# Optimization experiments

Measured on AMD Instinct MI355X. Metric: run time of the kernel, lower is better.

Reference implementation:

```python
import jax, jax.numpy as jnp
import numpy as np

B, S, H, F, E, TOPK = 2, 1024, 1024, 2816, 8, 2

def setup_inputs() -> dict:
    key = jax.random.key(0)
    k1, k2, k3, k4 = jax.random.split(key, 4)
    return {
        "hidden_states": jax.random.normal(k1, (B, S, H), dtype=jnp.float32),
        "gate_w": jax.random.normal(k2, (E, H), dtype=jnp.float32) * 0.02,  # gate 1x1 conv == [E,H] matrix
        "w1": jax.random.normal(k3, (E, F, H), dtype=jnp.float32) * 0.02,   # per-expert up-proj
        "w2": jax.random.normal(k4, (E, H, F), dtype=jnp.float32) * 0.02,   # per-expert down-proj
        "top_k": TOPK,
    }

def reference(hidden_states, gate_w, w1, w2, top_k):
    b, s, h = hidden_states.shape
    e = gate_w.shape[0]
    x = hidden_states.reshape(-1, h)                       # [N, H]
    n = x.shape[0]
    # Router: 1x1 conv gate == linear, softmax, top-k, renormalize
    logits = x @ gate_w.T                                  # [N, E]
    probs = jax.nn.softmax(logits, axis=-1)
    topw, topi = jax.lax.top_k(probs, top_k)               # [N, k]
    topw = topw / jnp.sum(topw, axis=-1, keepdims=True)
    # Per-(token, expert) combine weight; zero for non-selected experts.
    # Equivalent to torch.where(topk_indices == e, topk_weights, 0).sum(-1).
    comb = jnp.zeros((n, e), dtype=x.dtype).at[jnp.arange(n)[:, None], topi].add(topw)  # [N, E]
    # Expert MLPs (1x1 convs == GEMMs): up -> SiLU -> down, weighted combine.
    up = jnp.einsum('nh,efh->nef', x, w1)                  # [N, E, F]
    act = jax.nn.silu(up)
    out = jnp.einsum('nef,ehf->neh', act, w2)              # [N, E, H]
    y = jnp.einsum('ne,neh->nh', comb, out)                # weighted combine
    return y.reshape(b, s, h)
```

## Files before the change

kernel.cpp:

```cpp
#include <hip/hip_runtime.h>
#include <stdint.h>

#define N_TOK 2048
#define H_DIM 1024
#define F_DIM 2816
#define N_EXP 8
#define NSLOT (N_TOK * 2)

#define BK 64
#define KSPLIT 2
#define KHALF (F_DIM / KSPLIT)

#define N8_X (N_TOK * H_DIM / 8)
#define N8_W (N_EXP * F_DIM * H_DIM / 8)

typedef __attribute__((ext_vector_type(8))) short bf16x8;
typedef __attribute__((ext_vector_type(4))) float f32x4;

typedef __attribute__((address_space(1))) unsigned int gu32;
typedef __attribute__((address_space(3))) unsigned int lu32;

static __device__ __forceinline__ unsigned short f2bf(float f) {
    union { float f; unsigned u; } v; v.f = f;
    unsigned r = v.u + 0x7fffu + ((v.u >> 16) & 1u);
    return (unsigned short)(r >> 16);
}

static __device__ __forceinline__ void gload16(const unsigned short* g, unsigned short* l) {
    __builtin_amdgcn_global_load_lds((const gu32*)g, (lu32*)l, 16, 0, 0);
}

__global__ __launch_bounds__(256) void convert_all_kernel(
    const float* __restrict__ x, const float* __restrict__ w1, const float* __restrict__ w2,
    unsigned short* __restrict__ x_bf, unsigned short* __restrict__ w1_bf, unsigned short* __restrict__ w2_bf)
{
    const int total = N8_X + 2 * N8_W;
    int i = blockIdx.x * 256 + threadIdx.x;
    const int stride = gridDim.x * 256;
    for (; i < total; i += stride) {
        const float* src; unsigned short* dst; size_t k;
        if (i < N8_X)            { src = x;  dst = x_bf;  k = i; }
        else if (i < N8_X + N8_W){ src = w1; dst = w1_bf; k = i - N8_X; }
        else                     { src = w2; dst = w2_bf; k = i - N8_X - N8_W; }
        const float4 a = *(const float4*)(src + k * 8);
        const float4 b = *(const float4*)(src + k * 8 + 4);
        ushort4 lo, hi;
        lo.x = f2bf(a.x); lo.y = f2bf(a.y); lo.z = f2bf(a.z); lo.w = f2bf(a.w);
        hi.x = f2bf(b.x); hi.y = f2bf(b.y); hi.z = f2bf(b.z); hi.w = f2bf(b.w);
        uint4 out;
        out.x = (unsigned)lo.x | ((unsigned)lo.y << 16);
        out.y = (unsigned)lo.z | ((unsigned)lo.w << 16);
        out.z = (unsigned)hi.x | ((unsigned)hi.y << 16);
        out.w = (unsigned)hi.z | ((unsigned)hi.w << 16);
        *(uint4*)(dst + k * 8) = out;
    }
}

__global__ __launch_bounds__(256) void router_kernel(
    const float* __restrict__ x, const float* __restrict__ gate_w,
    int* __restrict__ counts, int* __restrict__ row_token, float* __restrict__ row_weight,
    int* __restrict__ slot_e, int* __restrict__ slot_pos)
{
    __shared__ float gsm[N_EXP * H_DIM];
    for (int i = threadIdx.x; i < N_EXP * H_DIM; i += 256) gsm[i] = gate_w[i];
    __syncthreads();

    const int wave = threadIdx.x >> 6;
    const int lane = threadIdx.x & 63;
    const int n = blockIdx.x * 4 + wave;
    if (n >= N_TOK) return;

    float xv[16];
#pragma unroll
    for (int i = 0; i < 16; i++) xv[i] = x[(size_t)n * H_DIM + lane + 64 * i];

    float logit[N_EXP];
#pragma unroll
    for (int e = 0; e < N_EXP; e++) {
        float p = 0.f;
#pragma unroll
        for (int i = 0; i < 16; i++) p += xv[i] * gsm[e * H_DIM + lane + 64 * i];
#pragma unroll
        for (int s = 32; s > 0; s >>= 1) p += __shfl_xor(p, s, 64);
        logit[e] = p;
    }

    if (lane == 0) {
        int e0 = 0; float l0 = logit[0];
#pragma unroll
        for (int e = 1; e < N_EXP; e++) if (logit[e] > l0) { l0 = logit[e]; e0 = e; }
        int e1 = -1; float l1 = -3.4e38f;
#pragma unroll
        for (int e = 0; e < N_EXP; e++) if (e != e0 && logit[e] > l1) { l1 = logit[e]; e1 = e; }
        float w0 = 1.f / (1.f + __expf(l1 - l0));
        float w1 = 1.f - w0;
        int p0 = atomicAdd(&counts[e0], 1);
        int p1 = atomicAdd(&counts[e1], 1);
        row_token[e0 * N_TOK + p0] = n;  row_weight[e0 * N_TOK + p0] = w0;
        row_token[e1 * N_TOK + p1] = n;  row_weight[e1 * N_TOK + p1] = w1;
        slot_e[n * 2 + 0] = e0;  slot_pos[n * 2 + 0] = p0;
        slot_e[n * 2 + 1] = e1;  slot_pos[n * 2 + 1] = p1;
    }
}

__global__ void scan_kernel(const int* __restrict__ counts, int* __restrict__ offsets)
{
    if (threadIdx.x == 0 && blockIdx.x == 0) {
        int acc = 0;
        for (int e = 0; e < N_EXP; e++) { offsets[e] = acc; acc += counts[e]; }
    }
}

__global__ __launch_bounds__(256) void up_gemm_kernel(
    const unsigned short* __restrict__ x_bf, const unsigned short* __restrict__ w1_bf,
    const int* __restrict__ counts, const int* __restrict__ offsets,
    const int* __restrict__ row_token,
    unsigned short* __restrict__ act)
{
    const int e = blockIdx.z;
    const int cnt = counts[e];
    const int mTile = blockIdx.y;
    if (mTile * 128 >= cnt) return;
    const int fTile = blockIdx.x;
    const int off = offsets[e];

    __shared__ __align__(16) unsigned short As[128 * 64];
    __shared__ __align__(16) unsigned short Bs[128 * 64];

    const int tid = threadIdx.x;
    const int lane = tid & 63;
    const int wave = tid >> 6;
    const int wm = (wave >> 1) * 64, wn = (wave & 1) * 64;

    const unsigned short* aSrc[4];
    const unsigned short* bSrc[4];
#pragma unroll
    for (int j = 0; j < 4; j++) {
        const int row_local = wave * 32 + j * 8 + (lane >> 3);
        const int pos = mTile * 128 + row_local;
        const int tok = row_token[e * N_TOK + min(pos, cnt - 1)];
        aSrc[j] = x_bf + (size_t)tok * H_DIM + (lane & 7) * 8;
        bSrc[j] = w1_bf + ((size_t)e * F_DIM + fTile * 128 + row_local) * H_DIM + (lane & 7) * 8;
    }

    f32x4 acc[4][4];
#pragma unroll
    for (int i = 0; i < 4; i++)
#pragma unroll
        for (int j = 0; j < 4; j++) acc[i][j] = (f32x4)(0.f);

    const int NKT = H_DIM / BK;
    for (int kt = 0; kt < NKT; kt++) {
        const int koff = kt * BK;
#pragma unroll
        for (int j = 0; j < 4; j++) {
            gload16(aSrc[j] + koff, As + (wave * 4 + j) * 512);
            gload16(bSrc[j] + koff, Bs + (wave * 4 + j) * 512);
        }
        __syncthreads();
#pragma unroll
        for (int kk = 0; kk < BK / 32; kk++) {
            const int kloc = kk * 32 + (lane >> 4) * 8;
            bf16x8 af[4], bfr[4];
#pragma unroll
            for (int i = 0; i < 4; i++)
                af[i] = *(const bf16x8*)(As + (wm + i * 16 + (lane & 15)) * 64 + kloc);
#pragma unroll
            for (int i = 0; i < 4; i++)
                bfr[i] = *(const bf16x8*)(Bs + (wn + i * 16 + (lane & 15)) * 64 + kloc);
#pragma unroll
            for (int i = 0; i < 4; i++)
#pragma unroll
                for (int j = 0; j < 4; j++)
                    acc[i][j] = __builtin_amdgcn_mfma_f32_16x16x32_bf16(af[i], bfr[j], acc[i][j], 0, 0, 0);
        }
        __syncthreads();
    }

#pragma unroll
    for (int i = 0; i < 4; i++) {
        const int mrow = wm + i * 16 + ((lane >> 4) << 2);
#pragma unroll
        for (int r = 0; r < 4; r++) {
            const int m = mTile * 128 + mrow + r;
            if (m < cnt) {
#pragma unroll
                for (int j = 0; j < 4; j++) {
                    float v = acc[i][j][r];
                    float s = v / (1.f + __expf(-v));
                    int col = fTile * 128 + wn + j * 16 + (lane & 15);
                    act[(size_t)(off + m) * F_DIM + col] = f2bf(s);
                }
            }
        }
    }
}

__global__ __launch_bounds__(256) void down_gemm_kernel(
    const unsigned short* __restrict__ act, const unsigned short* __restrict__ w2_bf,
    const int* __restrict__ counts, const int* __restrict__ offsets,
    const float* __restrict__ row_weight,
    float* __restrict__ out_partial)
{
    const int e  = blockIdx.z & (N_EXP - 1);
    const int ks = blockIdx.z >> 3;
    const int cnt = counts[e];
    const int mTile = blockIdx.y;
    if (mTile * 128 >= cnt) return;
    const int hTile = blockIdx.x;
    const int off = offsets[e];
    const int kbase = ks * KHALF;

    __shared__ __align__(16) unsigned short As[128 * 64];
    __shared__ __align__(16) unsigned short Bs[128 * 64];

    const int tid = threadIdx.x;
    const int lane = tid & 63;
    const int wave = tid >> 6;
    const int wm = (wave >> 1) * 64, wn = (wave & 1) * 64;

    const unsigned short* aSrc[4];
    const unsigned short* bSrc[4];
#pragma unroll
    for (int j = 0; j < 4; j++) {
        const int row_local = wave * 32 + j * 8 + (lane >> 3);
        const int slot = off + min(mTile * 128 + row_local, cnt - 1);
        aSrc[j] = act + (size_t)slot * F_DIM + kbase + (lane & 7) * 8;
        bSrc[j] = w2_bf + ((size_t)e * H_DIM + hTile * 128 + row_local) * F_DIM + kbase + (lane & 7) * 8;
    }

    f32x4 acc[4][4];
#pragma unroll
    for (int i = 0; i < 4; i++)
#pragma unroll
        for (int j = 0; j < 4; j++) acc[i][j] = (f32x4)(0.f);

    const int NKT = KHALF / BK;
    for (int kt = 0; kt < NKT; kt++) {
        const int koff = kt * BK;
#pragma unroll
        for (int j = 0; j < 4; j++) {
            gload16(aSrc[j] + koff, As + (wave * 4 + j) * 512);
            gload16(bSrc[j] + koff, Bs + (wave * 4 + j) * 512);
        }
        __syncthreads();
#pragma unroll
        for (int kk = 0; kk < BK / 32; kk++) {
            const int kloc = kk * 32 + (lane >> 4) * 8;
            bf16x8 af[4], bfr[4];
#pragma unroll
            for (int i = 0; i < 4; i++)
                af[i] = *(const bf16x8*)(As + (wm + i * 16 + (lane & 15)) * 64 + kloc);
#pragma unroll
            for (int i = 0; i < 4; i++)
                bfr[i] = *(const bf16x8*)(Bs + (wn + i * 16 + (lane & 15)) * 64 + kloc);
#pragma unroll
            for (int i = 0; i < 4; i++)
#pragma unroll
                for (int j = 0; j < 4; j++)
                    acc[i][j] = __builtin_amdgcn_mfma_f32_16x16x32_bf16(af[i], bfr[j], acc[i][j], 0, 0, 0);
        }
        __syncthreads();
    }

    float* obase = out_partial + (size_t)ks * NSLOT * H_DIM;
#pragma unroll
    for (int i = 0; i < 4; i++) {
        const int mrow = wm + i * 16 + ((lane >> 4) << 2);
#pragma unroll
        for (int r = 0; r < 4; r++) {
            const int m = mTile * 128 + mrow + r;
            if (m < cnt) {
                const float w = row_weight[e * N_TOK + m];
#pragma unroll
                for (int j = 0; j < 4; j++) {
                    int col = hTile * 128 + wn + j * 16 + (lane & 15);
                    obase[(size_t)(off + m) * H_DIM + col] = w * acc[i][j][r];
                }
            }
        }
    }
}

__global__ __launch_bounds__(256) void combine_kernel(
    const float* __restrict__ out_partial, const int* __restrict__ offsets,
    const int* __restrict__ slot_e, const int* __restrict__ slot_pos,
    float* __restrict__ out)
{
    const int n = blockIdx.x;
    const int r0 = offsets[slot_e[n * 2 + 0]] + slot_pos[n * 2 + 0];
    const int r1 = offsets[slot_e[n * 2 + 1]] + slot_pos[n * 2 + 1];
    const int t = threadIdx.x;
    const float* p0 = out_partial;
    const float* p1 = out_partial + (size_t)NSLOT * H_DIM;
    const float4 a = *(const float4*)(p0 + (size_t)r0 * H_DIM + t * 4);
    const float4 b = *(const float4*)(p1 + (size_t)r0 * H_DIM + t * 4);
    const float4 c = *(const float4*)(p0 + (size_t)r1 * H_DIM + t * 4);
    const float4 d = *(const float4*)(p1 + (size_t)r1 * H_DIM + t * 4);
    float4 s;
    s.x = (a.x + b.x) + (c.x + d.x);
    s.y = (a.y + b.y) + (c.y + d.y);
    s.z = (a.z + b.z) + (c.z + d.z);
    s.w = (a.w + b.w) + (c.w + d.w);
    *(float4*)(out + (size_t)n * H_DIM + t * 4) = s;
}

extern "C" void kernel_launch(void* const* d_in, const int* in_sizes, int n_in,
                              void* d_out, int out_size, void* d_ws, size_t ws_size,
                              hipStream_t stream) {
    const float* x      = (const float*)d_in[0];
    const float* gate_w = (const float*)d_in[1];
    const float* w1     = (const float*)d_in[2];
    const float* w2     = (const float*)d_in[3];
    float* out = (float*)d_out;

    char* ws = (char*)d_ws;
    size_t o = 0;
    auto alloc = [&](size_t bytes) -> void* {
        void* p = ws + o;
        o = (o + bytes + 255) & ~(size_t)255;
        return p;
    };
    int*   counts     = (int*)  alloc(N_EXP * sizeof(int));
    int*   offsets    = (int*)  alloc(N_EXP * sizeof(int));
    int*   row_token  = (int*)  alloc((size_t)N_EXP * N_TOK * sizeof(int));
    float* row_weight = (float*)alloc((size_t)N_EXP * N_TOK * sizeof(float));
    int*   slot_e     = (int*)  alloc((size_t)N_TOK * 2 * sizeof(int));
    int*   slot_pos   = (int*)  alloc((size_t)N_TOK * 2 * sizeof(int));
    unsigned short* act = (unsigned short*)alloc((size_t)NSLOT * F_DIM * sizeof(unsigned short));
    float* out_partial = (float*)alloc((size_t)KSPLIT * NSLOT * H_DIM * sizeof(float));
    unsigned short* x_bf  = (unsigned short*)alloc((size_t)N_TOK * H_DIM * sizeof(unsigned short));
    unsigned short* w1_bf = (unsigned short*)alloc((size_t)N_EXP * F_DIM * H_DIM * sizeof(unsigned short));
    unsigned short* w2_bf = (unsigned short*)alloc((size_t)N_EXP * H_DIM * F_DIM * sizeof(unsigned short));

    hipMemsetAsync(counts, 0, N_EXP * sizeof(int), stream);

    router_kernel<<<N_TOK / 4, 256, 0, stream>>>(x, gate_w, counts, row_token, row_weight, slot_e, slot_pos);
    scan_kernel<<<1, 64, 0, stream>>>(counts, offsets);
    convert_all_kernel<<<2048, 256, 0, stream>>>(x, w1, w2, x_bf, w1_bf, w2_bf);
    up_gemm_kernel<<<dim3(F_DIM / 128, N_TOK / 128, N_EXP), 256, 0, stream>>>(
        x_bf, w1_bf, counts, offsets, row_token, act);
    down_gemm_kernel<<<dim3(H_DIM / 128, N_TOK / 128, N_EXP * KSPLIT), 256, 0, stream>>>(
        act, w2_bf, counts, offsets, row_weight, out_partial);
    combine_kernel<<<N_TOK, 256, 0, stream>>>(out_partial, offsets, slot_e, slot_pos, out);
}
```

Baseline: 391.7 us.

## Fuse x bf16 conversion into router, swizzle GEMM tiles across XCDs

The router now writes the bf16 copy of x while it already holds the row in registers, and loads x and the gate weights as float4. The conversion kernel now handles only the weights, with two 8-element units per thread and a larger grid. The up and down GEMMs remap block indices so neighbouring tiles land on the same XCD for L2 reuse. Together these aim to cut redundant reads of x and conversion overhead. The swizzle also changes which mTile each block sees, so the early-exit pattern for empty tiles differs.

```diff
diff --git a/kernel.cpp b/kernel.cpp
--- a/kernel.cpp
+++ b/kernel.cpp
@@ -11,8 +11,7 @@
 #define KSPLIT 2
 #define KHALF (F_DIM / KSPLIT)
 
-#define N8_X (N_TOK * H_DIM / 8)
-#define N8_W (N_EXP * F_DIM * H_DIM / 8)
+#define NU_W (N_EXP * F_DIM * H_DIM / 8)
 
 typedef __attribute__((ext_vector_type(8))) short bf16x8;
 typedef __attribute__((ext_vector_type(4))) float f32x4;
@@ -30,39 +29,51 @@
     __builtin_amdgcn_global_load_lds((const gu32*)g, (lu32*)l, 16, 0, 0);
 }
 
-__global__ __launch_bounds__(256) void convert_all_kernel(
-    const float* __restrict__ x, const float* __restrict__ w1, const float* __restrict__ w2,
-    unsigned short* __restrict__ x_bf, unsigned short* __restrict__ w1_bf, unsigned short* __restrict__ w2_bf)
-{
-    const int total = N8_X + 2 * N8_W;
-    int i = blockIdx.x * 256 + threadIdx.x;
-    const int stride = gridDim.x * 256;
-    for (; i < total; i += stride) {
-        const float* src; unsigned short* dst; size_t k;
-        if (i < N8_X)            { src = x;  dst = x_bf;  k = i; }
-        else if (i < N8_X + N8_W){ src = w1; dst = w1_bf; k = i - N8_X; }
-        else                     { src = w2; dst = w2_bf; k = i - N8_X - N8_W; }
-        const float4 a = *(const float4*)(src + k * 8);
-        const float4 b = *(const float4*)(src + k * 8 + 4);
-        ushort4 lo, hi;
-        lo.x = f2bf(a.x); lo.y = f2bf(a.y); lo.z = f2bf(a.z); lo.w = f2bf(a.w);
-        hi.x = f2bf(b.x); hi.y = f2bf(b.y); hi.z = f2bf(b.z); hi.w = f2bf(b.w);
-        uint4 out;
-        out.x = (unsigned)lo.x | ((unsigned)lo.y << 16);
-        out.y = (unsigned)lo.z | ((unsigned)lo.w << 16);
-        out.z = (unsigned)hi.x | ((unsigned)hi.y << 16);
-        out.w = (unsigned)hi.z | ((unsigned)hi.w << 16);
-        *(uint4*)(dst + k * 8) = out;
+static __device__ __forceinline__ void xcd_swz(int gx, int nwg, int& bx, int& by) {
+    int f = bx + gx * by;
+    const int cpx = nwg >> 3;
+    f = (f & 7) * cpx + (f >> 3);
+    bx = f % gx; by = f / gx;
+}
+
+static __device__ __forceinline__ void conv8(const float* __restrict__ src,
+                                             unsigned short* __restrict__ dst, long k)
+{
+    const float4 a = *(const float4*)(src + k * 8);
+    const float4 b = *(const float4*)(src + k * 8 + 4);
+    uint4 o;
+    o.x = (unsigned)f2bf(a.x) | ((unsigned)f2bf(a.y) << 16);
+    o.y = (unsigned)f2bf(a.z) | ((unsigned)f2bf(a.w) << 16);
+    o.z = (unsigned)f2bf(b.x) | ((unsigned)f2bf(b.y) << 16);
+    o.w = (unsigned)f2bf(b.z) | ((unsigned)f2bf(b.w) << 16);
+    *(uint4*)(dst + k * 8) = o;
+}
+
+__global__ __launch_bounds__(256) void convert_w_kernel(
+    const float* __restrict__ w1, const float* __restrict__ w2,
+    unsigned short* __restrict__ w1_bf, unsigned short* __restrict__ w2_bf)
+{
+    const long total = 2L * NU_W;
+    long u = ((long)blockIdx.x * 256 + threadIdx.x) * 2;
+    const long stride = (long)gridDim.x * 256 * 2;
+    for (; u < total; u += stride) {
+        const float* src = (u < NU_W) ? w1 : w2;
+        unsigned short* dst = (u < NU_W) ? w1_bf : w2_bf;
+        const long k = (u < NU_W) ? u : u - NU_W;
+        conv8(src, dst, k);
+        conv8(src, dst, k + 1);
     }
 }
 
 __global__ __launch_bounds__(256) void router_kernel(
     const float* __restrict__ x, const float* __restrict__ gate_w,
     int* __restrict__ counts, int* __restrict__ row_token, float* __restrict__ row_weight,
-    int* __restrict__ slot_e, int* __restrict__ slot_pos)
+    int* __restrict__ slot_e, int* __restrict__ slot_pos,
+    unsigned short* __restrict__ x_bf)
 {
     __shared__ float gsm[N_EXP * H_DIM];
-    for (int i = threadIdx.x; i < N_EXP * H_DIM; i += 256) gsm[i] = gate_w[i];
+    for (int i = threadIdx.x; i < N_EXP * H_DIM / 4; i += 256)
+        ((float4*)gsm)[i] = ((const float4*)gate_w)[i];
     __syncthreads();
 
     const int wave = threadIdx.x >> 6;
@@ -70,16 +81,27 @@
     const int n = blockIdx.x * 4 + wave;
     if (n >= N_TOK) return;
 
-    float xv[16];
-#pragma unroll
-    for (int i = 0; i < 16; i++) xv[i] = x[(size_t)n * H_DIM + lane + 64 * i];
+    const float4* xrow = (const float4*)(x + (size_t)n * H_DIM);
+    float4 xv[4];
+#pragma unroll
+    for (int i = 0; i < 4; i++) xv[i] = xrow[lane + 64 * i];
+
+#pragma unroll
+    for (int i = 0; i < 4; i++) {
+        ushort4 b;
+        b.x = f2bf(xv[i].x); b.y = f2bf(xv[i].y); b.z = f2bf(xv[i].z); b.w = f2bf(xv[i].w);
+        *(ushort4*)(x_bf + (size_t)n * H_DIM + (lane + 64 * i) * 4) = b;
+    }
 
     float logit[N_EXP];
 #pragma unroll
     for (int e = 0; e < N_EXP; e++) {
         float p = 0.f;
 #pragma unroll
-        for (int i = 0; i < 16; i++) p += xv[i] * gsm[e * H_DIM + lane + 64 * i];
+        for (int i = 0; i < 4; i++) {
+            const float4 g = ((const float4*)gsm)[e * 256 + lane + 64 * i];
+            p += xv[i].x * g.x + xv[i].y * g.y + xv[i].z * g.z + xv[i].w * g.w;
+        }
 #pragma unroll
         for (int s = 32; s > 0; s >>= 1) p += __shfl_xor(p, s, 64);
         logit[e] = p;
@@ -119,9 +141,9 @@
 {
     const int e = blockIdx.z;
     const int cnt = counts[e];
-    const int mTile = blockIdx.y;
+    int fTile = blockIdx.x, mTile = blockIdx.y;
+    xcd_swz(F_DIM / 128, (F_DIM / 128) * (N_TOK / 128), fTile, mTile);
     if (mTile * 128 >= cnt) return;
-    const int fTile = blockIdx.x;
     const int off = offsets[e];
 
     __shared__ __align__(16) unsigned short As[128 * 64];
@@ -205,9 +227,9 @@
     const int e  = blockIdx.z & (N_EXP - 1);
     const int ks = blockIdx.z >> 3;
     const int cnt = counts[e];
-    const int mTile = blockIdx.y;
+    int hTile = blockIdx.x, mTile = blockIdx.y;
+    xcd_swz(H_DIM / 128, (H_DIM / 128) * (N_TOK / 128), hTile, mTile);
     if (mTile * 128 >= cnt) return;
-    const int hTile = blockIdx.x;
     const int off = offsets[e];
     const int kbase = ks * KHALF;
 
@@ -335,9 +357,9 @@
 
     hipMemsetAsync(counts, 0, N_EXP * sizeof(int), stream);
 
-    router_kernel<<<N_TOK / 4, 256, 0, stream>>>(x, gate_w, counts, row_token, row_weight, slot_e, slot_pos);
+    router_kernel<<<N_TOK / 4, 256, 0, stream>>>(x, gate_w, counts, row_token, row_weight, slot_e, slot_pos, x_bf);
     scan_kernel<<<1, 64, 0, stream>>>(counts, offsets);
-    convert_all_kernel<<<2048, 256, 0, stream>>>(x, w1, w2, x_bf, w1_bf, w2_bf);
+    convert_w_kernel<<<4096, 256, 0, stream>>>(w1, w2, w1_bf, w2_bf);
     up_gemm_kernel<<<dim3(F_DIM / 128, N_TOK / 128, N_EXP), 256, 0, stream>>>(
         x_bf, w1_bf, counts, offsets, row_token, act);
     down_gemm_kernel<<<dim3(H_DIM / 128, N_TOK / 128, N_EXP * KSPLIT), 256, 0, stream>>>(
```

New measurement: 571.4 us. 45.9% more time.
